# Kernel tuning notes

Hardware: AMD Instinct MI355X
Metric: run time of the kernel (lower is better)

## Reference

```python
import jax, jax.numpy as jnp
import numpy as np

# ---- constants derived from init_kwargs ----
DETECT_THRESHOLD = 3.0
DETECT_SIGN = -1          # negative spikes
MARGIN_LEFT = 20          # snippet_T1
MARGIN_RIGHT = 20         # snippet_T2
CHANNEL_RADIUS = 100.0
SAMPLING_FREQUENCY = 30000.0
TIME_RADIUS = int(np.ceil(0.5 / 1000.0 * SAMPLING_FREQUENCY))  # = 15
MAX_DETECTIONS = 100000   # static cap for jit-compatible compaction


def setup_inputs() -> dict:
    key = jax.random.key(0)
    k1, k2 = jax.random.split(key)
    traces = jax.random.normal(k1, (150000, 384), dtype=jnp.float32)
    # spread channels over a 2000x2000 um area so radius=100 gives sparse adjacency
    channel_locations = jax.random.uniform(k2, (384, 2), dtype=jnp.float32) * 2000.0
    return {"traces": traces, "channel_locations": channel_locations}


def _detect_mask(traces, channel_locations):
    N, M = traces.shape
    # orientation (detect_sign < 0 -> traces_inv = -traces)
    if DETECT_SIGN > 0:
        traces_inv = traces
    elif DETECT_SIGN == 0:
        traces_inv = jnp.abs(traces)
    else:
        traces_inv = -traces

    # temporal max-pool, kernel 2*TR+1, stride 1, same padding (pads with -inf)
    pool = 2 * TIME_RADIUS + 1
    neg_inf = jnp.float32(-jnp.inf)
    temporal_max = jax.lax.reduce_window(
        traces_inv, neg_inf, jax.lax.max,
        window_dimensions=(pool, 1), window_strides=(1, 1),
        padding=((TIME_RADIUS, TIME_RADIUS), (0, 0)))  # [N, M]

    # channel adjacency from pairwise distances
    diff = channel_locations[:, None, :] - channel_locations[None, :, :]
    dists = jnp.sqrt(jnp.sum(diff * diff, axis=-1))  # [M, M]
    adj = dists <= CHANNEL_RADIUS

    # per-channel masked neighbor max over temporal_max columns -> [N, M]
    # sequential lax.map over channels avoids an N x M x M intermediate
    spatial_max = jax.lax.map(
        lambda row: jnp.max(jnp.where(row[None, :], temporal_max, neg_inf), axis=1),
        adj).T  # [N, M]

    t = jnp.arange(N)
    margin_ok = (t >= MARGIN_LEFT) & (t < N - MARGIN_RIGHT)  # [N]

    valid = ((traces_inv == temporal_max)
             & (traces_inv >= DETECT_THRESHOLD)
             & margin_ok[:, None]
             & (traces_inv >= spatial_max))
    return valid, traces_inv


def reference(traces, channel_locations):
    valid, _ = _detect_mask(traces, channel_locations)
    # row-major nonzero order == stable sort by time (row index)
    times, chans = jnp.nonzero(valid, size=MAX_DETECTIONS, fill_value=-1)
    return times.astype(jnp.int64), chans.astype(jnp.int32)
```

## Files before the change

### kernel.cpp

```cpp
#include <hip/hip_runtime.h>
#include <stdint.h>

#define M_CH       384
#define TR         15
#define MARGIN     20
#define CHUNK_ROWS 16
#define BM_WORDS   192
#define WPR        12
#define WIN_ROWS   46

__device__ __forceinline__ uint32_t spread4(uint32_t x) {
    x = (x | (x << 12)) & 0x000F000Fu;
    x = (x | (x << 6))  & 0x03030303u;
    x = (x | (x << 3))  & 0x11111111u;
    return x;
}

__global__ __launch_bounds__(256)
void cand_kernel(const float* __restrict__ traces,
                 const float* __restrict__ locs,
                 long n4, long nwords, int nbrBlock,
                 uint32_t* __restrict__ candWords,
                 uint32_t* __restrict__ nEntries,
                 uint8_t* __restrict__ entryWord,
                 uint32_t* __restrict__ entryMask,
                 int maxdet, int* __restrict__ times, int* __restrict__ chans) {
    if ((int)blockIdx.x > nbrBlock) {
        int i = ((int)blockIdx.x - nbrBlock - 1) * 256 + threadIdx.x;
        if (i < maxdet) { times[i] = -1; chans[i] = -1; }
        return;
    }
    if ((int)blockIdx.x == nbrBlock) {
        __shared__ float lx[M_CH], ly[M_CH];
        const int t = threadIdx.x;
        for (int c = t; c < M_CH; c += 256) {
            lx[c] = locs[2 * c];
            ly[c] = locs[2 * c + 1];
        }
        __syncthreads();
        for (int c0 = t; c0 < M_CH; c0 += 256) {
            float x = lx[c0], y = ly[c0];
            int ne = 0;
            for (int k = 0; k < WPR; ++k) {
                uint32_t mk = 0;
                #pragma unroll
                for (int b = 0; b < 32; ++b) {
                    int c = k * 32 + b;
                    float dx = x - lx[c], dy = y - ly[c];
                    if (sqrtf(dx * dx + dy * dy) <= 100.0f) mk |= 1u << b;
                }
                if (mk) {
                    entryWord[c0 * WPR + ne] = (uint8_t)k;
                    entryMask[c0 * WPR + ne] = mk;
                    ne++;
                }
            }
            nEntries[c0] = (uint32_t)ne;
        }
        return;
    }

    const int lane = threadIdx.x & 63;
    const long wv = (((long)blockIdx.x * 256) + threadIdx.x) >> 6;
    const long fb = wv * 256;
    uint64_t B00,B01,B02,B03, B10,B11,B12,B13,
             B20,B21,B22,B23, B30,B31,B32,B33;
    {
        float4 v0 = make_float4(0,0,0,0), v1 = v0, v2 = v0, v3 = v0;
        long i0 = fb + 0 * 64 + lane;
        long i1 = fb + 1 * 64 + lane;
        long i2 = fb + 2 * 64 + lane;
        long i3 = fb + 3 * 64 + lane;
        if (i0 < n4) v0 = ((const float4*)traces)[i0];
        if (i1 < n4) v1 = ((const float4*)traces)[i1];
        if (i2 < n4) v2 = ((const float4*)traces)[i2];
        if (i3 < n4) v3 = ((const float4*)traces)[i3];
        B00 = __ballot(v0.x <= -3.0f); B01 = __ballot(v0.y <= -3.0f);
        B02 = __ballot(v0.z <= -3.0f); B03 = __ballot(v0.w <= -3.0f);
        B10 = __ballot(v1.x <= -3.0f); B11 = __ballot(v1.y <= -3.0f);
        B12 = __ballot(v1.z <= -3.0f); B13 = __ballot(v1.w <= -3.0f);
        B20 = __ballot(v2.x <= -3.0f); B21 = __ballot(v2.y <= -3.0f);
        B22 = __ballot(v2.z <= -3.0f); B23 = __ballot(v2.w <= -3.0f);
        B30 = __ballot(v3.x <= -3.0f); B31 = __ballot(v3.y <= -3.0f);
        B32 = __ballot(v3.z <= -3.0f); B33 = __ballot(v3.w <= -3.0f);
    }
    if (lane < 32) {
        int k  = lane >> 3;
        int sh = (lane & 7) * 8;
        uint64_t b0 = (k & 2) ? ((k & 1) ? B30 : B20) : ((k & 1) ? B10 : B00);
        uint64_t b1 = (k & 2) ? ((k & 1) ? B31 : B21) : ((k & 1) ? B11 : B01);
        uint64_t b2 = (k & 2) ? ((k & 1) ? B32 : B22) : ((k & 1) ? B12 : B02);
        uint64_t b3 = (k & 2) ? ((k & 1) ? B33 : B23) : ((k & 1) ? B13 : B03);
        uint32_t w = spread4((uint32_t)(b0 >> sh) & 0xFFu)
                   | (spread4((uint32_t)(b1 >> sh) & 0xFFu) << 1)
                   | (spread4((uint32_t)(b2 >> sh) & 0xFFu) << 2)
                   | (spread4((uint32_t)(b3 >> sh) & 0xFFu) << 3);
        long wIdx = wv * 32 + lane;
        if (wIdx < nwords) candWords[wIdx] = w;
    }
}

__global__ __launch_bounds__(192)
void validate_count_kernel(const float* __restrict__ traces, int N, long nwords,
                           const uint32_t* __restrict__ nEntries,
                           const uint8_t* __restrict__ entryWord,
                           const uint32_t* __restrict__ entryMask,
                           const uint32_t* __restrict__ candWords,
                           uint32_t* __restrict__ validOut,
                           uint32_t* __restrict__ chunkCounts) {
    __shared__ uint32_t win[WIN_ROWS * WPR];
    __shared__ uint32_t red[3];
    const int t = threadIdx.x;
    const int r0 = (int)blockIdx.x * CHUNK_ROWS;

    {
        const long gbase = (long)(r0 - TR) * WPR;
        #pragma unroll
        for (int i0 = 0; i0 < WIN_ROWS * WPR; i0 += 192) {
            int i = i0 + t;
            if (i < WIN_ROWS * WPR) {
                long g = gbase + i;
                win[i] = (g >= 0 && g < nwords) ? candWords[g] : 0u;
            }
        }
    }
    __syncthreads();

    const int lr = t / WPR;
    const int wi = t - lr * WPR;
    const int r  = r0 + lr;
    const long w = (long)blockIdx.x * BM_WORDS + t;

    uint32_t out = 0;
    if (w < nwords) {
        uint32_t word = win[(lr + TR) * WPR + wi];
        if (word && r >= MARGIN && r < N - MARGIN) {
            out = word;
            uint32_t tmp = word;
            while (tmp) {
                int bit = __ffs(tmp) - 1;
                tmp &= tmp - 1;
                const int c = wi * 32 + bit;
                const uint32_t selfbit = 1u << bit;
                const int ne = (int)nEntries[c];

                uint32_t anyComp = 0;
                for (int k = 0; k < ne; ++k) {
                    int wiE = (int)entryWord[c * WPR + k];
                    uint32_t em = entryMask[c * WPR + k];
                    const uint32_t* colp = &win[lr * WPR + wiE];
                    uint32_t orw = 0;
                    #pragma unroll
                    for (int dt = 0; dt < 31; ++dt) {
                        uint32_t h = colp[dt * WPR];
                        if (dt == TR) h &= (wiE == wi) ? ~selfbit : 0xFFFFFFFFu;
                        orw |= h & em;
                    }
                    anyComp |= orw;
                }

                if (anyComp) {
                    float raw = traces[(long)r * M_CH + c];
                    bool bad = false;
                    for (int k = 0; k < ne && !bad; ++k) {
                        int wiE = (int)entryWord[c * WPR + k];
                        uint32_t em = entryMask[c * WPR + k];
                        const uint32_t* colp = &win[lr * WPR + wiE];
                        #pragma unroll
                        for (int dt = 0; dt < 31; ++dt) {
                            uint32_t h = colp[dt * WPR] & em;
                            if (dt == TR && wiE == wi) h &= ~selfbit;
                            while (h) {
                                int b2 = __ffs(h) - 1;
                                h &= h - 1;
                                float v = traces[(long)(r - TR + dt) * M_CH + wiE * 32 + b2];
                                if (v < raw) bad = true;
                            }
                        }
                    }
                    if (bad) out &= ~selfbit;
                }
            }
        }
        validOut[w] = out;
    }
    int pc = __popc(out);
    #pragma unroll
    for (int off = 32; off; off >>= 1) pc += __shfl_xor(pc, off, 64);
    if ((t & 63) == 0) red[t >> 6] = (uint32_t)pc;
    __syncthreads();
    if (t == 0) chunkCounts[blockIdx.x] = red[0] + red[1] + red[2];
}

__global__ __launch_bounds__(256)
void emit_kernel(const uint32_t* __restrict__ validOut,
                 const uint32_t* __restrict__ chunkCounts,
                 int nchunk, int maxdet,
                 int* __restrict__ times, int* __restrict__ chans) {
    __shared__ uint32_t sred[4];
    __shared__ uint32_t cnts4[4];
    const int t = threadIdx.x;
    const int lane = t & 63;
    const int wv   = t >> 6;
    const int c0 = (int)blockIdx.x * 4;

    if (t < 4) cnts4[t] = (c0 + t < nchunk) ? chunkCounts[c0 + t] : 0u;

    uint32_t part = 0;
    for (int i = t; i < c0; i += 256) part += chunkCounts[i];
    #pragma unroll
    for (int off = 32; off; off >>= 1) part += __shfl_xor(part, off, 64);
    if (lane == 0) sred[wv] = part;
    __syncthreads();
    uint32_t base0 = sred[0] + sred[1] + sred[2] + sred[3];

    const int chunkId = c0 + wv;
    if (chunkId >= nchunk) return;
    uint32_t basePref = base0;
    #pragma unroll
    for (int k = 0; k < 3; ++k) if (k < wv) basePref += cnts4[k];

    const uint32_t* wp = validOut + (long)chunkId * BM_WORDS + lane * 3;
    uint32_t b0 = wp[0], b1 = wp[1], b2 = wp[2];
    int local = __popc(b0) + __popc(b1) + __popc(b2);

    int s = local;
    #pragma unroll
    for (int off = 1; off < 64; off <<= 1) {
        int v = __shfl_up(s, off, 64);
        if (lane >= off) s += v;
    }
    int base = (int)basePref + (s - local);
    int r0 = chunkId * CHUNK_ROWS;

    uint32_t words[3] = { b0, b1, b2 };
    #pragma unroll
    for (int q = 0; q < 3; ++q) {
        uint32_t x = words[q];
        int fbase = (lane * 3 + q) * 32;
        while (x) {
            int b = __ffs(x) - 1;
            x &= x - 1;
            int f = fbase + b;
            int n = f / M_CH;
            int ch = f - n * M_CH;
            if (base < maxdet) {
                times[base] = r0 + n;
                chans[base] = ch;
            }
            base++;
        }
    }
}

extern "C" void kernel_launch(void* const* d_in, const int* in_sizes, int n_in,
                              void* d_out, int out_size, void* d_ws, size_t ws_size,
                              hipStream_t stream) {
    const float* traces = (const float*)d_in[0];
    const float* locs   = (const float*)d_in[1];
    const int M = M_CH;
    const int N = in_sizes[0] / M;
    const long nsamp = (long)N * M;
    const int maxdet = out_size / 2;
    int* times = (int*)d_out;
    int* chans = times + maxdet;

    const long n4     = nsamp / 4;
    const long nwords = nsamp / 32;
    const int  nchunk = (N + CHUNK_ROWS - 1) / CHUNK_ROWS;

    char* ws = (char*)d_ws;
    uint32_t* nEntries    = (uint32_t*)(ws + 0);
    uint8_t*  entryWord   = (uint8_t*)(ws + 1536);
    uint32_t* entryMask   = (uint32_t*)(ws + 6144);
    uint32_t* chunkCounts = (uint32_t*)(ws + 24576);
    uint32_t* candWords   = (uint32_t*)(ws + 65536);
    uint32_t* validOut    = (uint32_t*)(ws + 7265536);

    const long nwaves = (nwords + 31) / 32;
    const int  cblocks = (int)((nwaves + 3) / 4);
    const int  fillBlocks = (maxdet + 255) / 256;
    cand_kernel<<<cblocks + 1 + fillBlocks, 256, 0, stream>>>(
        traces, locs, n4, nwords, cblocks,
        candWords, nEntries, entryWord, entryMask,
        maxdet, times, chans);

    validate_count_kernel<<<nchunk, BM_WORDS, 0, stream>>>(
        traces, N, nwords, nEntries, entryWord, entryMask, candWords,
        validOut, chunkCounts);

    const int emitBlocks = (nchunk + 3) / 4;
    emit_kernel<<<emitBlocks, 256, 0, stream>>>(
        validOut, chunkCounts, nchunk, maxdet, times, chans);
}
```

Measured before the change: 437.5 us.

## Fuse candidate bitmask construction into validate kernel, dropping global candWords buffer

Each validate block now reads its own 46-row window of traces, builds the threshold bitmask with ballots, and writes it straight into shared memory. This removes the separate pass that wrote the candidate bitmask to global memory and read it back. The cost is redundant traffic: each 16-row chunk reloads 46 rows, about 2.9x the trace reads. The adjacency setup and output fill move into a small init kernel.

```diff
diff --git a/kernel.cpp b/kernel.cpp
--- a/kernel.cpp
+++ b/kernel.cpp
@@ -8,6 +8,9 @@
 #define BM_WORDS   192
 #define WPR        12
 #define WIN_ROWS   46
+#define F4_PER_ROW 96
+
+typedef float vfloat4 __attribute__((ext_vector_type(4)));
 
 __device__ __forceinline__ uint32_t spread4(uint32_t x) {
     x = (x | (x << 12)) & 0x000F000Fu;
@@ -17,110 +20,95 @@
 }
 
 __global__ __launch_bounds__(256)
-void cand_kernel(const float* __restrict__ traces,
-                 const float* __restrict__ locs,
-                 long n4, long nwords, int nbrBlock,
-                 uint32_t* __restrict__ candWords,
+void init_kernel(const float* __restrict__ locs,
                  uint32_t* __restrict__ nEntries,
                  uint8_t* __restrict__ entryWord,
                  uint32_t* __restrict__ entryMask,
                  int maxdet, int* __restrict__ times, int* __restrict__ chans) {
-    if ((int)blockIdx.x > nbrBlock) {
-        int i = ((int)blockIdx.x - nbrBlock - 1) * 256 + threadIdx.x;
+    if ((int)blockIdx.x >= 1) {
+        int i = ((int)blockIdx.x - 1) * 256 + threadIdx.x;
         if (i < maxdet) { times[i] = -1; chans[i] = -1; }
         return;
     }
-    if ((int)blockIdx.x == nbrBlock) {
-        __shared__ float lx[M_CH], ly[M_CH];
-        const int t = threadIdx.x;
-        for (int c = t; c < M_CH; c += 256) {
-            lx[c] = locs[2 * c];
-            ly[c] = locs[2 * c + 1];
-        }
-        __syncthreads();
-        for (int c0 = t; c0 < M_CH; c0 += 256) {
-            float x = lx[c0], y = ly[c0];
-            int ne = 0;
-            for (int k = 0; k < WPR; ++k) {
-                uint32_t mk = 0;
-                #pragma unroll
-                for (int b = 0; b < 32; ++b) {
-                    int c = k * 32 + b;
-                    float dx = x - lx[c], dy = y - ly[c];
-                    if (sqrtf(dx * dx + dy * dy) <= 100.0f) mk |= 1u << b;
-                }
-                if (mk) {
-                    entryWord[c0 * WPR + ne] = (uint8_t)k;
-                    entryMask[c0 * WPR + ne] = mk;
-                    ne++;
-                }
-            }
-            nEntries[c0] = (uint32_t)ne;
-        }
-        return;
-    }
-
-    const int lane = threadIdx.x & 63;
-    const long wv = (((long)blockIdx.x * 256) + threadIdx.x) >> 6;
-    const long fb = wv * 256;
-    uint64_t B00,B01,B02,B03, B10,B11,B12,B13,
-             B20,B21,B22,B23, B30,B31,B32,B33;
-    {
-        float4 v0 = make_float4(0,0,0,0), v1 = v0, v2 = v0, v3 = v0;
-        long i0 = fb + 0 * 64 + lane;
-        long i1 = fb + 1 * 64 + lane;
-        long i2 = fb + 2 * 64 + lane;
-        long i3 = fb + 3 * 64 + lane;
-        if (i0 < n4) v0 = ((const float4*)traces)[i0];
-        if (i1 < n4) v1 = ((const float4*)traces)[i1];
-        if (i2 < n4) v2 = ((const float4*)traces)[i2];
-        if (i3 < n4) v3 = ((const float4*)traces)[i3];
-        B00 = __ballot(v0.x <= -3.0f); B01 = __ballot(v0.y <= -3.0f);
-        B02 = __ballot(v0.z <= -3.0f); B03 = __ballot(v0.w <= -3.0f);
-        B10 = __ballot(v1.x <= -3.0f); B11 = __ballot(v1.y <= -3.0f);
-        B12 = __ballot(v1.z <= -3.0f); B13 = __ballot(v1.w <= -3.0f);
-        B20 = __ballot(v2.x <= -3.0f); B21 = __ballot(v2.y <= -3.0f);
-        B22 = __ballot(v2.z <= -3.0f); B23 = __ballot(v2.w <= -3.0f);
-        B30 = __ballot(v3.x <= -3.0f); B31 = __ballot(v3.y <= -3.0f);
-        B32 = __ballot(v3.z <= -3.0f); B33 = __ballot(v3.w <= -3.0f);
-    }
-    if (lane < 32) {
-        int k  = lane >> 3;
-        int sh = (lane & 7) * 8;
-        uint64_t b0 = (k & 2) ? ((k & 1) ? B30 : B20) : ((k & 1) ? B10 : B00);
-        uint64_t b1 = (k & 2) ? ((k & 1) ? B31 : B21) : ((k & 1) ? B11 : B01);
-        uint64_t b2 = (k & 2) ? ((k & 1) ? B32 : B22) : ((k & 1) ? B12 : B02);
-        uint64_t b3 = (k & 2) ? ((k & 1) ? B33 : B23) : ((k & 1) ? B13 : B03);
-        uint32_t w = spread4((uint32_t)(b0 >> sh) & 0xFFu)
-                   | (spread4((uint32_t)(b1 >> sh) & 0xFFu) << 1)
-                   | (spread4((uint32_t)(b2 >> sh) & 0xFFu) << 2)
-                   | (spread4((uint32_t)(b3 >> sh) & 0xFFu) << 3);
-        long wIdx = wv * 32 + lane;
-        if (wIdx < nwords) candWords[wIdx] = w;
+    __shared__ float lx[M_CH], ly[M_CH];
+    const int t = threadIdx.x;
+    for (int c = t; c < M_CH; c += 256) {
+        lx[c] = locs[2 * c];
+        ly[c] = locs[2 * c + 1];
+    }
+    __syncthreads();
+    for (int c0 = t; c0 < M_CH; c0 += 256) {
+        float x = lx[c0], y = ly[c0];
+        int ne = 0;
+        for (int k = 0; k < WPR; ++k) {
+            uint32_t mk = 0;
+            #pragma unroll
+            for (int b = 0; b < 32; ++b) {
+                int c = k * 32 + b;
+                float dx = x - lx[c], dy = y - ly[c];
+                if (sqrtf(dx * dx + dy * dy) <= 100.0f) mk |= 1u << b;
+            }
+            if (mk) {
+                entryWord[c0 * WPR + ne] = (uint8_t)k;
+                entryMask[c0 * WPR + ne] = mk;
+                ne++;
+            }
+        }
+        nEntries[c0] = (uint32_t)ne;
     }
 }
 
 __global__ __launch_bounds__(192)
-void validate_count_kernel(const float* __restrict__ traces, int N, long nwords,
+void fused_validate_kernel(const float* __restrict__ traces, int N,
+                           long n4, long nwords,
                            const uint32_t* __restrict__ nEntries,
                            const uint8_t* __restrict__ entryWord,
                            const uint32_t* __restrict__ entryMask,
-                           const uint32_t* __restrict__ candWords,
                            uint32_t* __restrict__ validOut,
                            uint32_t* __restrict__ chunkCounts) {
     __shared__ uint32_t win[WIN_ROWS * WPR];
     __shared__ uint32_t red[3];
     const int t = threadIdx.x;
-    const int r0 = (int)blockIdx.x * CHUNK_ROWS;
+    const int lane = t & 63;
+    const int wv   = t >> 6;
+    const int bid  = (int)blockIdx.x;
+    const int r0   = bid * CHUNK_ROWS;
 
     {
-        const long gbase = (long)(r0 - TR) * WPR;
-        #pragma unroll
-        for (int i0 = 0; i0 < WIN_ROWS * WPR; i0 += 192) {
-            int i = i0 + t;
-            if (i < WIN_ROWS * WPR) {
-                long g = gbase + i;
-                win[i] = (g >= 0 && g < nwords) ? candWords[g] : 0u;
+        const long base4 = ((long)r0 - TR) * F4_PER_ROW;
+        const bool full = (r0 - TR >= 0) && (r0 + CHUNK_ROWS + TR <= N);
+        const int g  = lane >> 3;
+        const int sh = 8 * g;
+        if (full) {
+            #pragma unroll 4
+            for (int it = 0; it < 23; ++it) {
+                const int j = wv * 23 + it;
+                vfloat4 v = ((const vfloat4*)traces)[base4 + (long)j * 64 + lane];
+                uint64_t B0 = __ballot(v[0] <= -3.0f);
+                uint64_t B1 = __ballot(v[1] <= -3.0f);
+                uint64_t B2 = __ballot(v[2] <= -3.0f);
+                uint64_t B3 = __ballot(v[3] <= -3.0f);
+                uint32_t w = spread4((uint32_t)(B0 >> sh) & 0xFFu)
+                           | (spread4((uint32_t)(B1 >> sh) & 0xFFu) << 1)
+                           | (spread4((uint32_t)(B2 >> sh) & 0xFFu) << 2)
+                           | (spread4((uint32_t)(B3 >> sh) & 0xFFu) << 3);
+                if ((lane & 7) == 0) win[j * 8 + g] = w;
+            }
+        } else {
+            for (int it = 0; it < 23; ++it) {
+                const int j = wv * 23 + it;
+                const long gi = base4 + (long)j * 64 + lane;
+                vfloat4 v = (vfloat4)0.0f;
+                if (gi >= 0 && gi < n4) v = ((const vfloat4*)traces)[gi];
+                uint64_t B0 = __ballot(v[0] <= -3.0f);
+                uint64_t B1 = __ballot(v[1] <= -3.0f);
+                uint64_t B2 = __ballot(v[2] <= -3.0f);
+                uint64_t B3 = __ballot(v[3] <= -3.0f);
+                uint32_t w = spread4((uint32_t)(B0 >> sh) & 0xFFu)
+                           | (spread4((uint32_t)(B1 >> sh) & 0xFFu) << 1)
+                           | (spread4((uint32_t)(B2 >> sh) & 0xFFu) << 2)
+                           | (spread4((uint32_t)(B3 >> sh) & 0xFFu) << 3);
+                if ((lane & 7) == 0) win[j * 8 + g] = w;
             }
         }
     }
@@ -129,7 +117,7 @@
     const int lr = t / WPR;
     const int wi = t - lr * WPR;
     const int r  = r0 + lr;
-    const long w = (long)blockIdx.x * BM_WORDS + t;
+    const long w = (long)bid * BM_WORDS + t;
 
     uint32_t out = 0;
     if (w < nwords) {
@@ -274,19 +262,14 @@
     uint8_t*  entryWord   = (uint8_t*)(ws + 1536);
     uint32_t* entryMask   = (uint32_t*)(ws + 6144);
     uint32_t* chunkCounts = (uint32_t*)(ws + 24576);
-    uint32_t* candWords   = (uint32_t*)(ws + 65536);
-    uint32_t* validOut    = (uint32_t*)(ws + 7265536);
-
-    const long nwaves = (nwords + 31) / 32;
-    const int  cblocks = (int)((nwaves + 3) / 4);
-    const int  fillBlocks = (maxdet + 255) / 256;
-    cand_kernel<<<cblocks + 1 + fillBlocks, 256, 0, stream>>>(
-        traces, locs, n4, nwords, cblocks,
-        candWords, nEntries, entryWord, entryMask,
-        maxdet, times, chans);
-
-    validate_count_kernel<<<nchunk, BM_WORDS, 0, stream>>>(
-        traces, N, nwords, nEntries, entryWord, entryMask, candWords,
+    uint32_t* validOut    = (uint32_t*)(ws + 65536);
+
+    const int fillBlocks = (maxdet + 255) / 256;
+    init_kernel<<<1 + fillBlocks, 256, 0, stream>>>(
+        locs, nEntries, entryWord, entryMask, maxdet, times, chans);
+
+    fused_validate_kernel<<<nchunk, BM_WORDS, 0, stream>>>(
+        traces, N, n4, nwords, nEntries, entryWord, entryMask,
         validOut, chunkCounts);
 
     const int emitBlocks = (nchunk + 3) / 4;
```

After: 495.6 us. +13.3%, slower.
